# Kernel optimization log

Measured on AMD Instinct MI355X. Metric: run time of the kernel, lower is better.

## Reference

```python
import jax, jax.numpy as jnp
import numpy as np
import math


def setup_inputs() -> dict:
    key = jax.random.key(0)
    kq, kk, kv, kt, kd = jax.random.split(key, 5)
    B, L, H, E = 2, 2048, 16, 64
    return {
        "queries": jax.random.normal(kq, (B, L, H, E), dtype=jnp.float32),
        "keys": jax.random.normal(kk, (B, L, H, E), dtype=jnp.float32),
        "values": jax.random.normal(kv, (B, L, H, E), dtype=jnp.float32),
        "tau": jax.random.uniform(kt, (B, 1), dtype=jnp.float32),
        "delta": jax.random.normal(kd, (B, L), dtype=jnp.float32),
    }


def reference(queries, keys, values, tau, delta):
    # queries/keys/values: [B, L, H, E]; tau: [B,1]; delta: [B,S]
    B, L, H, E = queries.shape
    scale = 1.0 / math.sqrt(E)
    # scores: [B, H, L, S]; tau broadcasts [B,1,1,1], delta broadcasts [B,1,1,S]
    scores = (jnp.einsum('blhe,bshe->bhls', queries, keys)
              * tau[:, None, None, :]
              + delta[:, None, None, :])
    # causal mask (mask_flag=True, attn_mask=None path)
    causal = jnp.triu(jnp.ones((L, L), dtype=bool), k=1)
    scores = jnp.where(causal, -jnp.inf, scores)
    A = jax.nn.softmax(scale * scores, axis=-1)  # dropout p=0
    V = jnp.einsum('bhls,bshd->blhd', A, values)
    return V
```

## Files before the change

### kernel.cpp

```cpp
#include <hip/hip_runtime.h>
#include <math.h>

#define LL 2048
#define HH 16
#define EE 64
#define ROWSTR (HH*EE)
#define NBH 32
#define NT 16
#define SCALE 0.125f
#define LOG2E 1.4426950408889634f

using bf16x8 = __attribute__((ext_vector_type(8))) __bf16;
using f32x4  = __attribute__((ext_vector_type(4))) float;
using s16x4  = __attribute__((ext_vector_type(4))) short;

__device__ __forceinline__ unsigned pkbf(float lo, float hi) {
    unsigned l = __builtin_bit_cast(unsigned, lo) + 0x8000u;
    unsigned h = __builtin_bit_cast(unsigned, hi) + 0x8000u;
    return __builtin_amdgcn_perm(h, l, 0x07060302u);
}
__device__ __forceinline__ uint4 pack8(float4 a, float4 b) {
    uint4 u; u.x = pkbf(a.x, a.y); u.y = pkbf(a.z, a.w);
    u.z = pkbf(b.x, b.y); u.w = pkbf(b.z, b.w); return u;
}

#if __has_builtin(__builtin_amdgcn_mfma_f32_16x16x16_bf16)
using bf16x4 = __attribute__((ext_vector_type(4))) __bf16;
__device__ __forceinline__ f32x4 mfma16(s16x4 a, s16x4 b, f32x4 c) {
    return __builtin_amdgcn_mfma_f32_16x16x16_bf16(
        __builtin_bit_cast(bf16x4, a), __builtin_bit_cast(bf16x4, b), c, 0, 0, 0);
}
#else
__device__ __forceinline__ f32x4 mfma16(s16x4 a, s16x4 b, f32x4 c) {
    return __builtin_amdgcn_mfma_f32_16x16x16bf16_1k(a, b, c, 0, 0, 0);
}
#endif

__global__ __launch_bounds__(512, 4) void dsattn(
    const float* __restrict__ Qg, const float* __restrict__ Kg,
    const float* __restrict__ Vg, const float* __restrict__ taug,
    const float* __restrict__ dg, float* __restrict__ Og)
{
    __shared__ __align__(16) unsigned short Ks[2][64 * 64];
    __shared__ __align__(16) unsigned short Vt[2][64 * 64];

    const int tid  = threadIdx.x;
    const int w    = tid >> 6;
    const int lane = tid & 63;
    const int m    = lane & 15;
    const int quad = lane >> 4;

    const int bid = blockIdx.x;
    const int bh  = bid & (NBH - 1);
    const int g   = bid >> 5;
    const int tt  = (g < 8) ? (15 - g) : (g - 8);
    const int b   = bh >> 4;
    const int h   = bh & 15;

    const float qscale = taug[b] * (SCALE * LOG2E);
    const float dscale = SCALE * LOG2E;
    const int diag_st = 2 * tt + (w >> 2);
    const int thr = (w & 3) * 16 + m - quad * 4;

    bf16x8 qb[2];
    {
        const float* qp = Qg + ((size_t)(b * LL + tt * 128 + w * 16 + m) * HH + h) * EE + quad * 8;
        #pragma unroll
        for (int ch = 0; ch < 2; ++ch) {
            float4 f0 = *(const float4*)(qp + ch * 32);
            float4 f1 = *(const float4*)(qp + ch * 32 + 4);
            f0.x *= qscale; f0.y *= qscale; f0.z *= qscale; f0.w *= qscale;
            f1.x *= qscale; f1.y *= qscale; f1.z *= qscale; f1.w *= qscale;
            qb[ch] = __builtin_bit_cast(bf16x8, pack8(f0, f1));
        }
    }

    const int skey = tid >> 3, kc = tid & 7, se0 = (tid & 7) * 8;
    const int sv = (tid & 31) * 2, ve = (tid >> 5) * 4;
    const float* kbase = Kg + ((size_t)b * LL * HH + h) * EE;
    const float* vbase = Vg + ((size_t)b * LL * HH + h) * EE;
    const float* dbase = dg + b * LL;
    const int nst = 2 * tt + 2;

    float4 kr0, kr1, va, vb, dr0, dr1, dr2, dr3;
    {
        const float* kp = kbase + (size_t)skey * ROWSTR + se0;
        kr0 = ((const float4*)kp)[0]; kr1 = ((const float4*)kp)[1];
        const float* vp = vbase + (size_t)sv * ROWSTR + ve;
        va = *(const float4*)(vp); vb = *(const float4*)(vp + ROWSTR);
        const float* dp = dbase + quad * 4;
        dr0 = *(const float4*)(dp); dr1 = *(const float4*)(dp + 16);
        dr2 = *(const float4*)(dp + 32); dr3 = *(const float4*)(dp + 48);
    }

    f32x4 Oacc[4] = {};
    float l_ = 0.f;

    for (int st = 0; st < nst; ++st) {
        const int par = st & 1;
        unsigned short* KsP = Ks[par];
        unsigned short* VtP = Vt[par];

        *(uint4*)&KsP[skey * 64 + (kc ^ (skey & 7)) * 8] = pack8(kr0, kr1);
        {
            float ra[4] = {va.x, va.y, va.z, va.w};
            float rb[4] = {vb.x, vb.y, vb.z, vb.w};
            #pragma unroll
            for (int i = 0; i < 4; ++i) {
                const int e = ve + i;
                *(unsigned*)&VtP[e * 64 + (((sv >> 3) ^ (e & 7)) * 8) + (sv & 7)] = pkbf(ra[i], rb[i]);
            }
        }
        __syncthreads();

        f32x4 dvx[4];
        dvx[0] = f32x4{dr0.x * dscale, dr0.y * dscale, dr0.z * dscale, dr0.w * dscale};
        dvx[1] = f32x4{dr1.x * dscale, dr1.y * dscale, dr1.z * dscale, dr1.w * dscale};
        dvx[2] = f32x4{dr2.x * dscale, dr2.y * dscale, dr2.z * dscale, dr2.w * dscale};
        dvx[3] = f32x4{dr3.x * dscale, dr3.y * dscale, dr3.z * dscale, dr3.w * dscale};

        if (st + 1 < nst) {
            const int row = (st + 1) * 64;
            const float* kp = kbase + (size_t)(row + skey) * ROWSTR + se0;
            kr0 = ((const float4*)kp)[0]; kr1 = ((const float4*)kp)[1];
            const float* vp = vbase + (size_t)(row + sv) * ROWSTR + ve;
            va = *(const float4*)(vp); vb = *(const float4*)(vp + ROWSTR);
            const float* dp = dbase + row + quad * 4;
            dr0 = *(const float4*)(dp); dr1 = *(const float4*)(dp + 16);
            dr2 = *(const float4*)(dp + 32); dr3 = *(const float4*)(dp + 48);
        }

        if (st <= diag_st) {
            f32x4 S[4];
            #pragma unroll
            for (int n = 0; n < 4; ++n) {
                bf16x8 kf = *(const bf16x8*)&KsP[(16 * n + m) * 64 + (quad ^ (m & 7)) * 8];
                S[n] = __builtin_amdgcn_mfma_f32_16x16x32_bf16(kf, qb[0], dvx[n], 0, 0, 0);
            }
            #pragma unroll
            for (int n = 0; n < 4; ++n) {
                bf16x8 kf = *(const bf16x8*)&KsP[(16 * n + m) * 64 + ((quad + 4) ^ (m & 7)) * 8];
                S[n] = __builtin_amdgcn_mfma_f32_16x16x32_bf16(kf, qb[1], S[n], 0, 0, 0);
            }

            if (st == diag_st) {
                #pragma unroll
                for (int n = 0; n < 4; ++n)
                    #pragma unroll
                    for (int r = 0; r < 4; ++r)
                        if (16 * n + r > thr) S[n][r] = -INFINITY;
            }

            float rs[4];
            #pragma unroll
            for (int n = 0; n < 4; ++n) {
                float p0 = __builtin_amdgcn_exp2f(S[n][0]);
                float p1 = __builtin_amdgcn_exp2f(S[n][1]);
                float p2 = __builtin_amdgcn_exp2f(S[n][2]);
                float p3 = __builtin_amdgcn_exp2f(S[n][3]);
                S[n][0] = p0; S[n][1] = p1; S[n][2] = p2; S[n][3] = p3;
                rs[n] = (p0 + p1) + (p2 + p3);
            }
            l_ += (rs[0] + rs[1]) + (rs[2] + rs[3]);

            s16x4 pb[4];
            #pragma unroll
            for (int n = 0; n < 4; ++n) {
                uint2 u; u.x = pkbf(S[n][0], S[n][1]); u.y = pkbf(S[n][2], S[n][3]);
                pb[n] = __builtin_bit_cast(s16x4, u);
            }

            #pragma unroll
            for (int eb = 0; eb < 4; ++eb) {
                const int e = 16 * eb + m;
                s16x4 vf[4];
                #pragma unroll
                for (int n = 0; n < 4; ++n)
                    vf[n] = *(const s16x4*)&VtP[e * 64 + (((2 * n + (quad >> 1)) ^ (m & 7)) * 8) + (quad & 1) * 4];
                #pragma unroll
                for (int n = 0; n < 4; ++n)
                    Oacc[eb] = mfma16(vf[n], pb[n], Oacc[eb]);
            }
        }
    }

    {
        float lt = l_ + __shfl_xor(l_, 16);
        lt = lt + __shfl_xor(lt, 32);
        const float inv = __builtin_amdgcn_rcpf(lt);
        float* op = Og + ((size_t)(b * LL + tt * 128 + w * 16 + m) * HH + h) * EE + quad * 4;
        #pragma unroll
        for (int n = 0; n < 4; ++n) {
            float4 o = {Oacc[n][0] * inv, Oacc[n][1] * inv, Oacc[n][2] * inv, Oacc[n][3] * inv};
            *(float4*)(op + 16 * n) = o;
        }
    }
}

extern "C" void kernel_launch(void* const* d_in, const int* in_sizes, int n_in,
                              void* d_out, int out_size, void* d_ws, size_t ws_size,
                              hipStream_t stream) {
    const float* Q     = (const float*)d_in[0];
    const float* K     = (const float*)d_in[1];
    const float* V     = (const float*)d_in[2];
    const float* tau   = (const float*)d_in[3];
    const float* delta = (const float*)d_in[4];
    float* out = (float*)d_out;
    dsattn<<<dim3(NBH * NT), dim3(512), 0, stream>>>(Q, K, V, tau, delta, out);
}
```

Measured before the change: 137.0 us.

## Split causal KV range across two blocks per tile and add combine kernel

Each query tile's key/value range is divided into two halves processed by separate blocks, doubling the grid and halving the longest block's loop. Unnormalized partial outputs and row sums are written to workspace, and a second kernel sums them and normalizes. This targets low occupancy and tail imbalance of the causal grid, at the cost of extra global traffic for fp32 partials and a second launch. It falls back to the original single-pass kernel when workspace is too small.

```diff
diff --git a/kernel.cpp b/kernel.cpp
--- a/kernel.cpp
+++ b/kernel.cpp
@@ -9,6 +9,9 @@
 #define NT 16
 #define SCALE 0.125f
 #define LOG2E 1.4426950408889634f
+#define OSZ (2*LL*HH*EE)
+#define NL  (2*LL*HH)
+#define WS_NEED ((size_t)(2*OSZ + 2*NL) * 4)
 
 using bf16x8 = __attribute__((ext_vector_type(8))) __bf16;
 using f32x4  = __attribute__((ext_vector_type(4))) float;
@@ -36,10 +39,12 @@
 }
 #endif
 
+template<int SPLITMODE>
 __global__ __launch_bounds__(512, 4) void dsattn(
     const float* __restrict__ Qg, const float* __restrict__ Kg,
     const float* __restrict__ Vg, const float* __restrict__ taug,
-    const float* __restrict__ dg, float* __restrict__ Og)
+    const float* __restrict__ dg, float* __restrict__ Og,
+    float* __restrict__ ws)
 {
     __shared__ __align__(16) unsigned short Ks[2][64 * 64];
     __shared__ __align__(16) unsigned short Vt[2][64 * 64];
@@ -51,11 +56,21 @@
     const int quad = lane >> 4;
 
     const int bid = blockIdx.x;
-    const int bh  = bid & (NBH - 1);
-    const int g   = bid >> 5;
-    const int tt  = (g < 8) ? (15 - g) : (g - 8);
-    const int b   = bh >> 4;
-    const int h   = bh & 15;
+    int tt, bh, split;
+    if (SPLITMODE) {
+        tt = (NT - 1) - (bid >> 6);
+        bh = bid & 31;
+        split = (bid >> 5) & 1;
+    } else {
+        const int g = bid >> 5;
+        tt = (g < 8) ? (15 - g) : (g - 8);
+        bh = bid & 31;
+        split = 0;
+    }
+    const int b = bh >> 4;
+    const int h = bh & 15;
+    const int s_begin = (SPLITMODE && split) ? (tt + 1) : 0;
+    const int s_end   = (SPLITMODE && !split) ? (tt + 1) : (2 * tt + 2);
 
     const float qscale = taug[b] * (SCALE * LOG2E);
     const float dscale = SCALE * LOG2E;
@@ -80,15 +95,15 @@
     const float* kbase = Kg + ((size_t)b * LL * HH + h) * EE;
     const float* vbase = Vg + ((size_t)b * LL * HH + h) * EE;
     const float* dbase = dg + b * LL;
-    const int nst = 2 * tt + 2;
 
     float4 kr0, kr1, va, vb, dr0, dr1, dr2, dr3;
     {
-        const float* kp = kbase + (size_t)skey * ROWSTR + se0;
+        const int row = s_begin * 64;
+        const float* kp = kbase + (size_t)(row + skey) * ROWSTR + se0;
         kr0 = ((const float4*)kp)[0]; kr1 = ((const float4*)kp)[1];
-        const float* vp = vbase + (size_t)sv * ROWSTR + ve;
+        const float* vp = vbase + (size_t)(row + sv) * ROWSTR + ve;
         va = *(const float4*)(vp); vb = *(const float4*)(vp + ROWSTR);
-        const float* dp = dbase + quad * 4;
+        const float* dp = dbase + row + quad * 4;
         dr0 = *(const float4*)(dp); dr1 = *(const float4*)(dp + 16);
         dr2 = *(const float4*)(dp + 32); dr3 = *(const float4*)(dp + 48);
     }
@@ -96,7 +111,7 @@
     f32x4 Oacc[4] = {};
     float l_ = 0.f;
 
-    for (int st = 0; st < nst; ++st) {
+    for (int st = s_begin; st < s_end; ++st) {
         const int par = st & 1;
         unsigned short* KsP = Ks[par];
         unsigned short* VtP = Vt[par];
@@ -119,7 +134,7 @@
         dvx[2] = f32x4{dr2.x * dscale, dr2.y * dscale, dr2.z * dscale, dr2.w * dscale};
         dvx[3] = f32x4{dr3.x * dscale, dr3.y * dscale, dr3.z * dscale, dr3.w * dscale};
 
-        if (st + 1 < nst) {
+        if (st + 1 < s_end) {
             const int row = (st + 1) * 64;
             const float* kp = kbase + (size_t)(row + skey) * ROWSTR + se0;
             kr0 = ((const float4*)kp)[0]; kr1 = ((const float4*)kp)[1];
@@ -187,14 +202,43 @@
     {
         float lt = l_ + __shfl_xor(l_, 16);
         lt = lt + __shfl_xor(lt, 32);
-        const float inv = __builtin_amdgcn_rcpf(lt);
-        float* op = Og + ((size_t)(b * LL + tt * 128 + w * 16 + m) * HH + h) * EE + quad * 4;
-        #pragma unroll
-        for (int n = 0; n < 4; ++n) {
-            float4 o = {Oacc[n][0] * inv, Oacc[n][1] * inv, Oacc[n][2] * inv, Oacc[n][3] * inv};
-            *(float4*)(op + 16 * n) = o;
-        }
-    }
+        const int q = tt * 128 + w * 16 + m;
+        if (SPLITMODE) {
+            float* Opw = ws + (size_t)split * OSZ
+                       + ((size_t)(b * LL + q) * HH + h) * EE + quad * 4;
+            #pragma unroll
+            for (int n = 0; n < 4; ++n) {
+                float4 o = {Oacc[n][0], Oacc[n][1], Oacc[n][2], Oacc[n][3]};
+                *(float4*)(Opw + 16 * n) = o;
+            }
+            if (quad == 0)
+                ws[(size_t)2 * OSZ + (size_t)split * NL + (size_t)(b * LL + q) * HH + h] = lt;
+        } else {
+            const float inv = __builtin_amdgcn_rcpf(lt);
+            float* op = Og + ((size_t)(b * LL + q) * HH + h) * EE + quad * 4;
+            #pragma unroll
+            for (int n = 0; n < 4; ++n) {
+                float4 o = {Oacc[n][0] * inv, Oacc[n][1] * inv, Oacc[n][2] * inv, Oacc[n][3] * inv};
+                *(float4*)(op + 16 * n) = o;
+            }
+        }
+    }
+}
+
+__global__ __launch_bounds__(256) void dscombine(
+    const float* __restrict__ ws, float* __restrict__ out)
+{
+    const int gid = blockIdx.x * 256 + threadIdx.x;
+    const float4* O0 = (const float4*)ws;
+    const float4* O1 = (const float4*)(ws + OSZ);
+    const float* l0 = ws + (size_t)2 * OSZ;
+    const float* l1 = l0 + NL;
+    const int j = gid >> 4;
+    const float inv = __builtin_amdgcn_rcpf(l0[j] + l1[j]);
+    float4 a = O0[gid], c = O1[gid];
+    float4 o = {(a.x + c.x) * inv, (a.y + c.y) * inv,
+                (a.z + c.z) * inv, (a.w + c.w) * inv};
+    ((float4*)out)[gid] = o;
 }
 
 extern "C" void kernel_launch(void* const* d_in, const int* in_sizes, int n_in,
@@ -206,5 +250,11 @@
     const float* tau   = (const float*)d_in[3];
     const float* delta = (const float*)d_in[4];
     float* out = (float*)d_out;
-    dsattn<<<dim3(NBH * NT), dim3(512), 0, stream>>>(Q, K, V, tau, delta, out);
-}
+    float* ws  = (float*)d_ws;
+    if (ws_size >= WS_NEED) {
+        dsattn<1><<<dim3(2 * NBH * NT), dim3(512), 0, stream>>>(Q, K, V, tau, delta, out, ws);
+        dscombine<<<dim3(OSZ / 4 / 256), dim3(256), 0, stream>>>(ws, out);
+    } else {
+        dsattn<0><<<dim3(NBH * NT), dim3(512), 0, stream>>>(Q, K, V, tau, delta, out, ws);
+    }
+}
```

New measurement: 142.0 us. 1.04x slower.

## Pre-convert K/V to swizzled bf16 tiles and stream them via global_load_lds

Applied to the files above, without the earlier changes.

Adds a prep kernel that converts K and V into bf16, pre-swizzled (and for V, transposed) 64x64 tile images in workspace, and pre-scales delta. The attention kernel then copies these tiles straight into LDS with global_load_lds double buffering, instead of loading fp32 into registers and converting and packing on every tile. This removes redundant per-block conversion work and register pressure, and it halves K/V bytes in the main loop. The cost is an extra kernel launch and a full extra pass writing and reading the workspace. It falls back to the old kernel if the workspace is too small.

```diff
diff --git a/kernel.cpp b/kernel.cpp
--- a/kernel.cpp
+++ b/kernel.cpp
@@ -7,8 +7,13 @@
 #define ROWSTR (HH*EE)
 #define NBH 32
 #define NT 16
+#define NST 32
 #define SCALE 0.125f
 #define LOG2E 1.4426950408889634f
+#define TILE_SH 4096
+#define KPRE_OFF 4096
+#define TILES_TOTAL ((size_t)NBH * NST)
+#define WS_NEED (16384ull + 2ull * TILES_TOTAL * TILE_SH * 2ull)
 
 using bf16x8 = __attribute__((ext_vector_type(8))) __bf16;
 using f32x4  = __attribute__((ext_vector_type(4))) float;
@@ -36,7 +41,216 @@
 }
 #endif
 
-__global__ __launch_bounds__(512, 4) void dsattn(
+__device__ __forceinline__ void gl_lds16(const void* g, void* l) {
+    __builtin_amdgcn_global_load_lds(
+        (const __attribute__((address_space(1))) unsigned int*)(unsigned long long)g,
+        (__attribute__((address_space(3))) unsigned int*)(unsigned long long)l,
+        16, 0, 0);
+}
+
+__global__ __launch_bounds__(256) void dsprep(
+    const float* __restrict__ K, const float* __restrict__ V,
+    const float* __restrict__ delta, float* __restrict__ ws)
+{
+    const int bid = blockIdx.x;
+    const int t = threadIdx.x;
+    float* dsc = ws;
+    unsigned short* kpre = (unsigned short*)(ws + KPRE_OFF);
+    unsigned short* vpre = kpre + TILES_TOTAL * TILE_SH;
+
+    if (bid >= NBH * NST) {
+        const int i = (bid - NBH * NST) * 256 + t;
+        dsc[i] = delta[i] * (SCALE * LOG2E);
+        return;
+    }
+    const int bh = bid & 31, st = bid >> 5;
+    const int b = bh >> 4, h = bh & 15;
+
+    unsigned short* kimg = kpre + ((size_t)bh * NST + st) * TILE_SH;
+    #pragma unroll
+    for (int i = 0; i < 2; ++i) {
+        const int slot = t + i * 256;
+        const int k = slot >> 3, c = slot & 7;
+        const float* src = K + ((size_t)(b * LL + st * 64 + k) * HH + h) * EE + c * 8;
+        float4 a = ((const float4*)src)[0], bq = ((const float4*)src)[1];
+        *(uint4*)&kimg[k * 64 + (c ^ (k & 7)) * 8] = pack8(a, bq);
+    }
+
+    __shared__ float vt[64 * 65];
+    {
+        const int s = t >> 2, seg = (t & 3) * 16;
+        const float* src = V + ((size_t)(b * LL + st * 64 + s) * HH + h) * EE + seg;
+        #pragma unroll
+        for (int i = 0; i < 4; ++i) {
+            float4 f = ((const float4*)src)[i];
+            vt[s * 65 + seg + 4 * i + 0] = f.x;
+            vt[s * 65 + seg + 4 * i + 1] = f.y;
+            vt[s * 65 + seg + 4 * i + 2] = f.z;
+            vt[s * 65 + seg + 4 * i + 3] = f.w;
+        }
+    }
+    __syncthreads();
+    {
+        unsigned short* vimg = vpre + ((size_t)bh * NST + st) * TILE_SH;
+        const int e = t >> 2, g = t & 3;
+        unsigned u[8];
+        #pragma unroll
+        for (int A = 0; A < 4; ++A) {
+            float x0 = vt[(16 * A + 4 * g + 0) * 65 + e];
+            float x1 = vt[(16 * A + 4 * g + 1) * 65 + e];
+            float x2 = vt[(16 * A + 4 * g + 2) * 65 + e];
+            float x3 = vt[(16 * A + 4 * g + 3) * 65 + e];
+            u[2 * A]     = pkbf(x0, x1);
+            u[2 * A + 1] = pkbf(x2, x3);
+        }
+        *(uint4*)&vimg[e * 64 + ((2 * g)     ^ (e & 7)) * 8] = uint4{u[0], u[1], u[2], u[3]};
+        *(uint4*)&vimg[e * 64 + ((2 * g + 1) ^ (e & 7)) * 8] = uint4{u[4], u[5], u[6], u[7]};
+    }
+}
+
+__global__ __launch_bounds__(512, 4) void dsattn_dma(
+    const float* __restrict__ Qg, const float* __restrict__ taug,
+    const float* __restrict__ ws_, float* __restrict__ Og)
+{
+    __shared__ __align__(16) unsigned short Ks[2][TILE_SH];
+    __shared__ __align__(16) unsigned short Vt[2][TILE_SH];
+
+    const int tid  = threadIdx.x;
+    const int w    = tid >> 6;
+    const int lane = tid & 63;
+    const int m    = lane & 15;
+    const int quad = lane >> 4;
+
+    const int bid = blockIdx.x;
+    const int bh  = bid & (NBH - 1);
+    const int g   = bid >> 5;
+    const int tt  = (g < 8) ? (15 - g) : (g - 8);
+    const int b   = bh >> 4;
+    const int h   = bh & 15;
+
+    const float* dsc = ws_;
+    const unsigned short* kpre = (const unsigned short*)(ws_ + KPRE_OFF);
+    const unsigned short* vpre = kpre + TILES_TOTAL * TILE_SH;
+    const unsigned short* ktiles = kpre + (size_t)bh * NST * TILE_SH;
+    const unsigned short* vtiles = vpre + (size_t)bh * NST * TILE_SH;
+
+    const float qscale = taug[b] * (SCALE * LOG2E);
+    const int diag_st = 2 * tt + (w >> 2);
+    const int thr = (w & 3) * 16 + m - quad * 4;
+
+    bf16x8 qb[2];
+    {
+        const float* qp = Qg + ((size_t)(b * LL + tt * 128 + w * 16 + m) * HH + h) * EE + quad * 8;
+        #pragma unroll
+        for (int ch = 0; ch < 2; ++ch) {
+            float4 f0 = *(const float4*)(qp + ch * 32);
+            float4 f1 = *(const float4*)(qp + ch * 32 + 4);
+            f0.x *= qscale; f0.y *= qscale; f0.z *= qscale; f0.w *= qscale;
+            f1.x *= qscale; f1.y *= qscale; f1.z *= qscale; f1.w *= qscale;
+            qb[ch] = __builtin_bit_cast(bf16x8, pack8(f0, f1));
+        }
+    }
+
+    const int nst = 2 * tt + 2;
+    const float* dbase = dsc + b * LL + quad * 4;
+
+    gl_lds16(ktiles + tid * 8, &Ks[0][w * 512]);
+    gl_lds16(vtiles + tid * 8, &Vt[0][w * 512]);
+
+    f32x4 Oacc[4] = {};
+    float l_ = 0.f;
+
+    for (int st = 0; st < nst; ++st) {
+        const int par = st & 1;
+        const unsigned short* KsP = Ks[par];
+        const unsigned short* VtP = Vt[par];
+
+        __syncthreads();
+
+        if (st + 1 < nst) {
+            gl_lds16(ktiles + (st + 1) * TILE_SH + tid * 8, &Ks[par ^ 1][w * 512]);
+            gl_lds16(vtiles + (st + 1) * TILE_SH + tid * 8, &Vt[par ^ 1][w * 512]);
+        }
+
+        if (st <= diag_st) {
+            const float* dp = dbase + st * 64;
+            float4 dr0 = *(const float4*)(dp);
+            float4 dr1 = *(const float4*)(dp + 16);
+            float4 dr2 = *(const float4*)(dp + 32);
+            float4 dr3 = *(const float4*)(dp + 48);
+
+            f32x4 S[4];
+            S[0] = __builtin_bit_cast(f32x4, dr0);
+            S[1] = __builtin_bit_cast(f32x4, dr1);
+            S[2] = __builtin_bit_cast(f32x4, dr2);
+            S[3] = __builtin_bit_cast(f32x4, dr3);
+            #pragma unroll
+            for (int n = 0; n < 4; ++n) {
+                bf16x8 kf = *(const bf16x8*)&KsP[(16 * n + m) * 64 + (quad ^ (m & 7)) * 8];
+                S[n] = __builtin_amdgcn_mfma_f32_16x16x32_bf16(kf, qb[0], S[n], 0, 0, 0);
+            }
+            #pragma unroll
+            for (int n = 0; n < 4; ++n) {
+                bf16x8 kf = *(const bf16x8*)&KsP[(16 * n + m) * 64 + ((quad + 4) ^ (m & 7)) * 8];
+                S[n] = __builtin_amdgcn_mfma_f32_16x16x32_bf16(kf, qb[1], S[n], 0, 0, 0);
+            }
+
+            if (st == diag_st) {
+                #pragma unroll
+                for (int n = 0; n < 4; ++n)
+                    #pragma unroll
+                    for (int r = 0; r < 4; ++r)
+                        if (16 * n + r > thr) S[n][r] = -INFINITY;
+            }
+
+            float rs[4];
+            #pragma unroll
+            for (int n = 0; n < 4; ++n) {
+                float p0 = __builtin_amdgcn_exp2f(S[n][0]);
+                float p1 = __builtin_amdgcn_exp2f(S[n][1]);
+                float p2 = __builtin_amdgcn_exp2f(S[n][2]);
+                float p3 = __builtin_amdgcn_exp2f(S[n][3]);
+                S[n][0] = p0; S[n][1] = p1; S[n][2] = p2; S[n][3] = p3;
+                rs[n] = (p0 + p1) + (p2 + p3);
+            }
+            l_ += (rs[0] + rs[1]) + (rs[2] + rs[3]);
+
+            s16x4 pb[4];
+            #pragma unroll
+            for (int n = 0; n < 4; ++n) {
+                uint2 u; u.x = pkbf(S[n][0], S[n][1]); u.y = pkbf(S[n][2], S[n][3]);
+                pb[n] = __builtin_bit_cast(s16x4, u);
+            }
+
+            #pragma unroll
+            for (int eb = 0; eb < 4; ++eb) {
+                const int e = 16 * eb + m;
+                uint4 r0 = *(const uint4*)&VtP[e * 64 + ((2 * quad)     ^ (m & 7)) * 8];
+                uint4 r1 = *(const uint4*)&VtP[e * 64 + ((2 * quad + 1) ^ (m & 7)) * 8];
+                f32x4 o = Oacc[eb];
+                o = mfma16(__builtin_bit_cast(s16x4, uint2{r0.x, r0.y}), pb[0], o);
+                o = mfma16(__builtin_bit_cast(s16x4, uint2{r0.z, r0.w}), pb[1], o);
+                o = mfma16(__builtin_bit_cast(s16x4, uint2{r1.x, r1.y}), pb[2], o);
+                o = mfma16(__builtin_bit_cast(s16x4, uint2{r1.z, r1.w}), pb[3], o);
+                Oacc[eb] = o;
+            }
+        }
+    }
+
+    {
+        float lt = l_ + __shfl_xor(l_, 16);
+        lt = lt + __shfl_xor(lt, 32);
+        const float inv = __builtin_amdgcn_rcpf(lt);
+        float* op = Og + ((size_t)(b * LL + tt * 128 + w * 16 + m) * HH + h) * EE + quad * 4;
+        #pragma unroll
+        for (int n = 0; n < 4; ++n) {
+            float4 o = {Oacc[n][0] * inv, Oacc[n][1] * inv, Oacc[n][2] * inv, Oacc[n][3] * inv};
+            *(float4*)(op + 16 * n) = o;
+        }
+    }
+}
+
+__global__ __launch_bounds__(512, 4) void dsattn_reg(
     const float* __restrict__ Qg, const float* __restrict__ Kg,
     const float* __restrict__ Vg, const float* __restrict__ taug,
     const float* __restrict__ dg, float* __restrict__ Og)
@@ -142,7 +356,6 @@
                 bf16x8 kf = *(const bf16x8*)&KsP[(16 * n + m) * 64 + ((quad + 4) ^ (m & 7)) * 8];
                 S[n] = __builtin_amdgcn_mfma_f32_16x16x32_bf16(kf, qb[1], S[n], 0, 0, 0);
             }
-
             if (st == diag_st) {
                 #pragma unroll
                 for (int n = 0; n < 4; ++n)
@@ -150,7 +363,6 @@
                     for (int r = 0; r < 4; ++r)
                         if (16 * n + r > thr) S[n][r] = -INFINITY;
             }
-
             float rs[4];
             #pragma unroll
             for (int n = 0; n < 4; ++n) {
@@ -169,7 +381,6 @@
                 uint2 u; u.x = pkbf(S[n][0], S[n][1]); u.y = pkbf(S[n][2], S[n][3]);
                 pb[n] = __builtin_bit_cast(s16x4, u);
             }
-
             #pragma unroll
             for (int eb = 0; eb < 4; ++eb) {
                 const int e = 16 * eb + m;
@@ -206,5 +417,11 @@
     const float* tau   = (const float*)d_in[3];
     const float* delta = (const float*)d_in[4];
     float* out = (float*)d_out;
-    dsattn<<<dim3(NBH * NT), dim3(512), 0, stream>>>(Q, K, V, tau, delta, out);
-}
+    float* ws  = (float*)d_ws;
+    if (ws_size >= WS_NEED) {
+        dsprep<<<dim3(NBH * NST + 16), dim3(256), 0, stream>>>(K, V, delta, ws);
+        dsattn_dma<<<dim3(NBH * NT), dim3(512), 0, stream>>>(Q, tau, ws, out);
+    } else {
+        dsattn_reg<<<dim3(NBH * NT), dim3(512), 0, stream>>>(Q, K, V, tau, delta, out);
+    }
+}
```

Result: no change. 135.4 us (-1.1%).
